# Optimization experiments

Measured on AMD Instinct MI355X. Metric: run time of the kernel, lower is better.

The kernel has to match this reference:

```python
import jax, jax.numpy as jnp
import numpy as np
from jax import lax

C = 256      # in_c == out_c == dim
NH = 8       # num_heads
K = 7        # depthwise pos-enc kernel
H1 = 512     # int(mlp_ratio * in_c) = 2.0 * 256
B, Hs, Ws = 2, 48, 48


def setup_inputs() -> dict:
    key = jax.random.key(0)
    ks = jax.random.split(key, 8)
    w = lambda k, shape: jax.random.normal(k, shape, jnp.float32) * 0.02
    return {
        "x": jax.random.normal(ks[0], (B, C, Hs, Ws), jnp.float32),
        # 1x1 convs stored as [out, in] (BN folded into weight+bias)
        "qk_w": w(ks[1], (2 * C, C)), "qk_b": jnp.zeros((2 * C,), jnp.float32),
        "v_w": w(ks[2], (C, C)),       "v_b": jnp.zeros((C,), jnp.float32),
        # depthwise positional encoding conv [C,1,K,K]
        "pe_w": w(ks[3], (C, 1, K, K)), "pe_b": jnp.zeros((C,), jnp.float32),
        "proj_w": w(ks[4], (C, C)),    "proj_b": jnp.zeros((C,), jnp.float32),
        # conv FFN: 1x1 (SiLU) -> 1x1 (no act)
        "fc1_w": w(ks[5], (H1, C)),    "fc1_b": jnp.zeros((H1,), jnp.float32),
        "fc2_w": w(ks[6], (C, H1)),    "fc2_b": jnp.zeros((C,), jnp.float32),
    }


def _c1(x, w, b):
    # 1x1 conv == per-pixel matmul
    return jnp.einsum('bchw,oc->bohw', x, w) + b[None, :, None, None]


def reference(x, qk_w, qk_b, v_w, v_b, pe_w, pe_b, proj_w, proj_b,
              fc1_w, fc1_b, fc2_w, fc2_b):
    Bb, Cc, Hh, Ww = x.shape
    hd = Cc // NH                 # head_dim = 32
    N = Hh * Ww
    scale = hd ** -0.5

    # ---- AttentionV2 ----
    qk = _c1(x, qk_w, qk_b).reshape(Bb, NH, 2 * hd, N)
    q, k = qk[:, :, :hd], qk[:, :, hd:]
    v_full = _c1(x, v_w, v_b)                      # [B,C,H,W]
    pe = lax.conv_general_dilated(
        v_full, pe_w, (1, 1), 'SAME', feature_group_count=Cc,
        dimension_numbers=('NCHW', 'OIHW', 'NCHW')) + pe_b[None, :, None, None]
    v = v_full.reshape(Bb, NH, hd, N)

    # attn = q^T @ k * scale ; softmax over keys
    attn = jax.nn.softmax(jnp.einsum('bhdn,bhdm->bhnm', q, k) * scale, axis=-1)
    o = jnp.einsum('bhdm,bhnm->bhdn', v, attn).reshape(Bb, Cc, Hh, Ww)
    attn_out = _c1(o + pe, proj_w, proj_b)

    # ---- block residuals + conv FFN (add=True) ----
    x1 = x + attn_out
    h = jax.nn.silu(_c1(x1, fc1_w, fc1_b))         # Conv(in_c, hidden, 1, 1) with SiLU
    return x1 + _c1(h, fc2_w, fc2_b)               # Conv(hidden, out_c, 1, act=False)
```

## Files before the change

### kernel.cpp

```cpp
#include <hip/hip_runtime.h>
#include <hip/hip_bf16.h>

#define NCH 256
#define NHD 8
#define HD 32
#define NPIX 2304
#define H1DIM 512

typedef __attribute__((ext_vector_type(8))) __bf16 bf16x8;
typedef __attribute__((ext_vector_type(4))) float f32x4;

__global__ __launch_bounds__(256) void prep_k(
    const float* __restrict__ x,
    const float* __restrict__ w0, const float* __restrict__ w1,
    const float* __restrict__ w2, const float* __restrict__ w3,
    const float* __restrict__ w4,
    __bf16* __restrict__ Xb, __bf16* __restrict__ Wall) {
    const int tid = threadIdx.x;
    if (blockIdx.x < 288) {
        const int t = blockIdx.x;
        const int b = t / 144, r0 = t % 144;
        const int c0 = (r0 / 36) * 64, n0 = (r0 % 36) * 64;
        __shared__ float tile[64][65];
        const size_t sb = ((size_t)b * NCH + c0) * NPIX + n0;
#pragma unroll
        for (int i = 0; i < 16; ++i) {
            int idx = tid + i * 256;
            int rr = idx >> 6, cc = idx & 63;
            tile[rr][cc] = x[sb + (size_t)rr * NPIX + cc];
        }
        __syncthreads();
#pragma unroll
        for (int i = 0; i < 8; ++i) {
            int idx = tid + i * 256;
            int nn = idx >> 5, cp = (idx & 31) * 2;
            union { __bf16 h[2]; unsigned u; } pk;
            pk.h[0] = (__bf16)tile[cp][nn];
            pk.h[1] = (__bf16)tile[cp + 1][nn];
            *(unsigned*)&Xb[((size_t)b * NPIX + n0 + nn) * NCH + c0 + cp] = pk.u;
        }
    } else {
        int i = (blockIdx.x - 288) * 256 + tid;
        const float* src; int off;
        if (i < 32768)      { src = w0; off = i; }
        else if (i < 49152) { src = w1; off = i - 32768; }
        else if (i < 65536) { src = w2; off = i - 49152; }
        else if (i < 98304) { src = w3; off = i - 65536; }
        else                { src = w4; off = i - 98304; }
        float4 v = ((const float4*)src)[off];
        union { __bf16 h[4]; uint2 u; } pk;
        pk.h[0] = (__bf16)v.x; pk.h[1] = (__bf16)v.y;
        pk.h[2] = (__bf16)v.z; pk.h[3] = (__bf16)v.w;
        ((uint2*)Wall)[i] = pk.u;
    }
}

__global__ __launch_bounds__(256) void qkv_k(
    const __bf16* __restrict__ A, const __bf16* __restrict__ Wq,
    const __bf16* __restrict__ Wv, const float* __restrict__ qk_b,
    const float* __restrict__ v_b, __bf16* __restrict__ Qb,
    __bf16* __restrict__ Kf, float* __restrict__ v_bu,
    __bf16* __restrict__ Vf) {
    const int tid = threadIdx.x;
    const int wave = tid >> 6, lane = tid & 63;
    const int l16 = lane & 15, quad = lane >> 4;
    const int h = blockIdx.x & 7;
    const int u = blockIdx.x >> 3;
    const int tau = u * 4 + wave;
    const int px = tau % 144;
    const int rest = tau / 144;
    const int b = rest & 1;
    const int sub = rest >> 1;
    const int m0 = px * 16;
    const bool isv = sub >= 4;
    const int oc0 = isv ? (32 * h + 16 * (sub - 4)) : (64 * h + 16 * sub);
    const __bf16* W = isv ? Wv : Wq;

    const __bf16* aptr = A + ((size_t)b * NPIX + m0 + l16) * NCH + quad * 8;
    const __bf16* bptr = W + (size_t)(oc0 + l16) * NCH + quad * 8;

    f32x4 acc = {0.f, 0.f, 0.f, 0.f};
#pragma unroll 8
    for (int k = 0; k < NCH; k += 32) {
        bf16x8 af = *(const bf16x8*)(aptr + k);
        bf16x8 bf = *(const bf16x8*)(bptr + k);
        acc = __builtin_amdgcn_mfma_f32_16x16x32_bf16(af, bf, acc, 0, 0, 0);
    }

    const int oc = oc0 + l16;
    const int mb = m0 + quad * 4;

    if (!isv) {
        const float bb = qk_b[oc];
        const int bh = b * NHD + h;
        const int dd = (oc0 & 16) + l16;
        if ((oc0 & 32) == 0) {
            const float qs = 0.17677669529663689f * 1.4426950408889634f;
#pragma unroll
            for (int r = 0; r < 4; ++r)
                Qb[((size_t)bh * NPIX + mb + r) * 32 + dd] = (__bf16)((acc[r] + bb) * qs);
        } else {
            __bf16* kp = Kf + ((size_t)(bh * 144 + px) * 64 + (dd >> 3) * 16 + quad * 4) * 8 + (dd & 7);
#pragma unroll
            for (int r = 0; r < 4; ++r) kp[r * 8] = (__bf16)(acc[r] + bb);
        }
    } else {
        const float bb = v_b[oc];
        const int bh = b * NHD + h;
        const int half = (oc0 >> 4) & 1;
        const size_t fb = ((size_t)b * NCH + oc) * NPIX + mb;
        float4 vf_; float* vp = &vf_.x;
        union { __bf16 hh[4]; uint2 u; } pk;
#pragma unroll
        for (int r = 0; r < 4; ++r) {
            float v = acc[r] + bb;
            vp[r] = v; pk.hh[r] = (__bf16)v;
        }
        *(float4*)&v_bu[fb] = vf_;
        *(uint2*)&Vf[((size_t)(bh * 144 + px) * 64 + lane) * 8 + half * 4] = pk.u;
    }
}

__global__ __launch_bounds__(256) void attn9_k(const __bf16* __restrict__ Qb,
                                               const __bf16* __restrict__ Kf,
                                               const __bf16* __restrict__ Vf,
                                               const float* __restrict__ v_bu,
                                               const float* __restrict__ pe_w,
                                               const float* __restrict__ pe_b,
                                               __bf16* __restrict__ opb) {
    const int tid = threadIdx.x;
    const int wave = tid >> 6, lane = tid & 63;
    const int l16 = lane & 15, quad = lane >> 4;
    const int h = blockIdx.x & 7;
    const int r0 = (int)blockIdx.x >> 3;
    const int qt = r0 % 72;
    const int b = r0 / 72;
    const int qb = qt * 32;
    const int bh = b * NHD + h;

    __shared__ float o_s[4][32][33];
    __shared__ float l_s[4][32];

    bf16x8 b_q0 = *(const bf16x8*)(Qb + ((size_t)bh * NPIX + qb + l16) * 32 + quad * 8);
    bf16x8 b_q1 = *(const bf16x8*)(Qb + ((size_t)bh * NPIX + qb + 16 + l16) * 32 + quad * 8);

    const __bf16* kf = Kf + ((size_t)(bh * 144 + wave * 36) * 64 + lane) * 8;
    const __bf16* vf = Vf + ((size_t)(bh * 144 + wave * 36) * 64 + lane) * 8;

    f32x4 o00 = {0.f,0.f,0.f,0.f}, o01 = {0.f,0.f,0.f,0.f};
    f32x4 o10 = {0.f,0.f,0.f,0.f}, o11 = {0.f,0.f,0.f,0.f};
    f32x4 l0 = {0.f,0.f,0.f,0.f}, l1 = {0.f,0.f,0.f,0.f};

#pragma unroll 3
    for (int t = 0; t < 36; ++t) {
        bf16x8 a_k = *(const bf16x8*)(kf + (size_t)t * 512);
        bf16x8 va  = *(const bf16x8*)(vf + (size_t)t * 512);
        f32x4 z = {0.f, 0.f, 0.f, 0.f};
        __builtin_amdgcn_s_setprio(1);
        f32x4 s0 = __builtin_amdgcn_mfma_f32_16x16x32_bf16(a_k, b_q0, z, 0, 0, 0);
        f32x4 s1 = __builtin_amdgcn_mfma_f32_16x16x32_bf16(a_k, b_q1, z, 0, 0, 0);
        __builtin_amdgcn_s_setprio(0);
        f32x4 p0, p1;
#pragma unroll
        for (int r = 0; r < 4; ++r) {
            p0[r] = __builtin_amdgcn_exp2f(s0[r]);
            p1[r] = __builtin_amdgcn_exp2f(s1[r]);
        }
        l0 += p0; l1 += p1;
        bf16x8 b0lo = {}, b0hi = {}, b1lo = {}, b1hi = {};
#pragma unroll
        for (int r = 0; r < 4; ++r) {
            __bf16 c0 = (__bf16)p0[r], c1 = (__bf16)p1[r];
            b0lo[r] = c0; b0hi[4 + r] = c0;
            b1lo[r] = c1; b1hi[4 + r] = c1;
        }
        __builtin_amdgcn_s_setprio(1);
        o00 = __builtin_amdgcn_mfma_f32_16x16x32_bf16(va, b0lo, o00, 0, 0, 0);
        o01 = __builtin_amdgcn_mfma_f32_16x16x32_bf16(va, b0hi, o01, 0, 0, 0);
        o10 = __builtin_amdgcn_mfma_f32_16x16x32_bf16(va, b1lo, o10, 0, 0, 0);
        o11 = __builtin_amdgcn_mfma_f32_16x16x32_bf16(va, b1hi, o11, 0, 0, 0);
        __builtin_amdgcn_s_setprio(0);
    }

    float ls0 = l0[0] + l0[1] + l0[2] + l0[3];
    ls0 += __shfl_xor(ls0, 16); ls0 += __shfl_xor(ls0, 32);
    float ls1 = l1[0] + l1[1] + l1[2] + l1[3];
    ls1 += __shfl_xor(ls1, 16); ls1 += __shfl_xor(ls1, 32);

#pragma unroll
    for (int r = 0; r < 4; ++r) {
        o_s[wave][quad * 4 + r][l16]           = o00[r];
        o_s[wave][16 + quad * 4 + r][l16]      = o01[r];
        o_s[wave][quad * 4 + r][16 + l16]      = o10[r];
        o_s[wave][16 + quad * 4 + r][16 + l16] = o11[r];
    }
    if (quad == 0) { l_s[wave][l16] = ls0; l_s[wave][16 + l16] = ls1; }
    __syncthreads();

    const int q = tid & 31;
    const int d0 = (tid >> 5) * 4;
    float l = l_s[0][q] + l_s[1][q] + l_s[2][q] + l_s[3][q];
    const float inv = 1.f / l;
    float v[4] = {0.f, 0.f, 0.f, 0.f};
#pragma unroll
    for (int w = 0; w < 4; ++w) {
#pragma unroll
        for (int j = 0; j < 4; ++j) v[j] += o_s[w][d0 + j][q];
    }
    const int n = qb + q;
    const int ch = h * HD + d0;

    const int y = n / 48, x0 = n - y * 48;
    const size_t vb0 = ((size_t)b * NCH + ch) * NPIX;
    float pe[4];
#pragma unroll
    for (int j = 0; j < 4; ++j) pe[j] = pe_b[ch + j];
#pragma unroll
    for (int ky = 0; ky < 7; ++ky) {
        int yy = y + ky - 3;
        if ((unsigned)yy < 48u) {
#pragma unroll
            for (int kx = 0; kx < 7; ++kx) {
                int xx = x0 + kx - 3;
                if ((unsigned)xx < 48u) {
                    const int off = yy * 48 + xx;
                    const int wko = ky * 7 + kx;
#pragma unroll
                    for (int j = 0; j < 4; ++j)
                        pe[j] += pe_w[(ch + j) * 49 + wko] * v_bu[vb0 + (size_t)j * NPIX + off];
                }
            }
        }
    }

    union { __bf16 hh[4]; uint2 u; } pk;
#pragma unroll
    for (int j = 0; j < 4; ++j) pk.hh[j] = (__bf16)(v[j] * inv + pe[j]);
    *(uint2*)&opb[((size_t)b * NPIX + n) * NCH + ch] = pk.u;
}

__global__ __launch_bounds__(512, 2) void mlp_k(
    const __bf16* __restrict__ opb, const __bf16* __restrict__ Wp,
    const __bf16* __restrict__ W1, const __bf16* __restrict__ W2,
    const float* __restrict__ pj_b, const float* __restrict__ f1_b,
    const float* __restrict__ f2_b, const float* __restrict__ x,
    float* __restrict__ out) {
    const int tid = threadIdx.x;
    const int wave = tid >> 6, lane = tid & 63;
    const int l16 = lane & 15, quad = lane >> 4;
    const int b = (int)blockIdx.x / 144;
    const int m0 = ((int)blockIdx.x % 144) * 16;

    __shared__ __bf16 x1h[16][264];
    __shared__ __bf16 hh[16][520];

    const int oc_a = wave * 16 + l16;
    const int oc_b = oc_a + 128;
    const int row = quad * 4;
    const int mq = m0 + quad * 4;

    const __bf16* aptr = opb + ((size_t)b * NPIX + m0 + l16) * NCH + quad * 8;
    const __bf16* wp0 = Wp + (size_t)oc_a * NCH + quad * 8;
    const __bf16* wp1 = Wp + (size_t)oc_b * NCH + quad * 8;
    f32x4 a0 = {0.f, 0.f, 0.f, 0.f}, a1 = {0.f, 0.f, 0.f, 0.f};
#pragma unroll
    for (int k = 0; k < NCH; k += 32) {
        bf16x8 af = *(const bf16x8*)(aptr + k);
        a0 = __builtin_amdgcn_mfma_f32_16x16x32_bf16(af, *(const bf16x8*)(wp0 + k), a0, 0, 0, 0);
        a1 = __builtin_amdgcn_mfma_f32_16x16x32_bf16(af, *(const bf16x8*)(wp1 + k), a1, 0, 0, 0);
    }
    float x1r0[4], x1r1[4];
    {
        const float bb0 = pj_b[oc_a], bb1 = pj_b[oc_b];
        float4 xr0 = *(const float4*)&x[((size_t)b * NCH + oc_a) * NPIX + mq];
        float4 xr1 = *(const float4*)&x[((size_t)b * NCH + oc_b) * NPIX + mq];
        const float* xp0 = &xr0.x;
        const float* xp1 = &xr1.x;
#pragma unroll
        for (int r = 0; r < 4; ++r) {
            float v0 = a0[r] + bb0 + xp0[r];
            float v1 = a1[r] + bb1 + xp1[r];
            x1r0[r] = v0; x1r1[r] = v1;
            x1h[row + r][oc_a] = (__bf16)v0;
            x1h[row + r][oc_b] = (__bf16)v1;
        }
    }
    __syncthreads();

    {
        const __bf16* w10 = W1 + (size_t)oc_a * NCH + quad * 8;
        const __bf16* w11 = W1 + (size_t)(oc_a + 128) * NCH + quad * 8;
        const __bf16* w12 = W1 + (size_t)(oc_a + 256) * NCH + quad * 8;
        const __bf16* w13 = W1 + (size_t)(oc_a + 384) * NCH + quad * 8;
        f32x4 c0 = {0.f, 0.f, 0.f, 0.f}, c1 = {0.f, 0.f, 0.f, 0.f};
        f32x4 c2 = {0.f, 0.f, 0.f, 0.f}, c3 = {0.f, 0.f, 0.f, 0.f};
#pragma unroll
        for (int k = 0; k < NCH; k += 32) {
            bf16x8 af = *(const bf16x8*)&x1h[l16][quad * 8 + k];
            c0 = __builtin_amdgcn_mfma_f32_16x16x32_bf16(af, *(const bf16x8*)(w10 + k), c0, 0, 0, 0);
            c1 = __builtin_amdgcn_mfma_f32_16x16x32_bf16(af, *(const bf16x8*)(w11 + k), c1, 0, 0, 0);
            c2 = __builtin_amdgcn_mfma_f32_16x16x32_bf16(af, *(const bf16x8*)(w12 + k), c2, 0, 0, 0);
            c3 = __builtin_amdgcn_mfma_f32_16x16x32_bf16(af, *(const bf16x8*)(w13 + k), c3, 0, 0, 0);
        }
        const float g0 = f1_b[oc_a], g1 = f1_b[oc_a + 128];
        const float g2 = f1_b[oc_a + 256], g3 = f1_b[oc_a + 384];
#pragma unroll
        for (int r = 0; r < 4; ++r) {
            float v0 = c0[r] + g0; v0 = v0 / (1.f + __expf(-v0));
            float v1 = c1[r] + g1; v1 = v1 / (1.f + __expf(-v1));
            float v2 = c2[r] + g2; v2 = v2 / (1.f + __expf(-v2));
            float v3 = c3[r] + g3; v3 = v3 / (1.f + __expf(-v3));
            hh[row + r][oc_a]       = (__bf16)v0;
            hh[row + r][oc_a + 128] = (__bf16)v1;
            hh[row + r][oc_a + 256] = (__bf16)v2;
            hh[row + r][oc_a + 384] = (__bf16)v3;
        }
    }
    __syncthreads();

    {
        const __bf16* w20 = W2 + (size_t)oc_a * H1DIM + quad * 8;
        const __bf16* w21 = W2 + (size_t)oc_b * H1DIM + quad * 8;
        f32x4 d0 = {0.f, 0.f, 0.f, 0.f}, d1 = {0.f, 0.f, 0.f, 0.f};
#pragma unroll
        for (int k = 0; k < H1DIM; k += 32) {
            bf16x8 af = *(const bf16x8*)&hh[l16][quad * 8 + k];
            d0 = __builtin_amdgcn_mfma_f32_16x16x32_bf16(af, *(const bf16x8*)(w20 + k), d0, 0, 0, 0);
            d1 = __builtin_amdgcn_mfma_f32_16x16x32_bf16(af, *(const bf16x8*)(w21 + k), d1, 0, 0, 0);
        }
        const float g0 = f2_b[oc_a], g1 = f2_b[oc_b];
        float4 o0, o1;
        float* p0 = &o0.x; float* p1 = &o1.x;
#pragma unroll
        for (int r = 0; r < 4; ++r) {
            p0[r] = d0[r] + g0 + x1r0[r];
            p1[r] = d1[r] + g1 + x1r1[r];
        }
        *(float4*)&out[((size_t)b * NCH + oc_a) * NPIX + mq] = o0;
        *(float4*)&out[((size_t)b * NCH + oc_b) * NPIX + mq] = o1;
    }
}

extern "C" void kernel_launch(void* const* d_in, const int* in_sizes, int n_in,
                              void* d_out, int out_size, void* d_ws, size_t ws_size,
                              hipStream_t stream) {
    const float* x    = (const float*)d_in[0];
    const float* qk_w = (const float*)d_in[1];
    const float* qk_b = (const float*)d_in[2];
    const float* v_w  = (const float*)d_in[3];
    const float* v_b  = (const float*)d_in[4];
    const float* pe_w = (const float*)d_in[5];
    const float* pe_b = (const float*)d_in[6];
    const float* pj_w = (const float*)d_in[7];
    const float* pj_b = (const float*)d_in[8];
    const float* f1_w = (const float*)d_in[9];
    const float* f1_b = (const float*)d_in[10];
    const float* f2_w = (const float*)d_in[11];
    const float* f2_b = (const float*)d_in[12];
    float* out = (float*)d_out;

    const int B = 2;
    const size_t plane = (size_t)NCH * NPIX;
    const size_t bp = (size_t)B * plane;

    float* v_bu  = (float*)d_ws;
    __bf16* Xb   = (__bf16*)(v_bu + bp);
    __bf16* opb  = Xb + bp;
    __bf16* Qb   = opb + bp;
    __bf16* Kf   = Qb + bp;
    __bf16* Vf   = Kf + bp;
    __bf16* Wall = Vf + bp;
    __bf16* Wq = Wall;
    __bf16* Wv = Wall + 131072;
    __bf16* Wp = Wall + 196608;
    __bf16* W1 = Wall + 262144;
    __bf16* W2 = Wall + 393216;

    prep_k<<<800, 256, 0, stream>>>(x, qk_w, v_w, pj_w, f1_w, f2_w, Xb, Wall);
    qkv_k<<<3456, 256, 0, stream>>>(Xb, Wq, Wv, qk_b, v_b, Qb, Kf, v_bu, Vf);
    attn9_k<<<1152, 256, 0, stream>>>(Qb, Kf, Vf, v_bu, pe_w, pe_b, opb);
    mlp_k<<<288, 512, 0, stream>>>(opb, Wp, W1, W2, pj_b, f1_b, f2_b, x, out);
}
```

Baseline: 190.0 us.

## Fuse input transpose and bf16 conversion into QKV projection kernel

Removes the separate prep kernel that transposed x into a pixel-major bf16 buffer. The QKV MFMA kernel now reads fp32 x and the fp32 qk/v weights directly, converting to bf16 in registers. Extra blocks appended to the same launch convert only the proj/fc1/fc2 weights for the MLP kernel. This saves a launch and an intermediate round trip, but the x loads are now strided by NPIX per element (16 consecutive pixels per lane group) and weights are re-read and re-converted redundantly by many blocks.

```diff
diff --git a/kernel.cpp b/kernel.cpp
--- a/kernel.cpp
+++ b/kernel.cpp
@@ -10,58 +10,29 @@
 typedef __attribute__((ext_vector_type(8))) __bf16 bf16x8;
 typedef __attribute__((ext_vector_type(4))) float f32x4;
 
-__global__ __launch_bounds__(256) void prep_k(
-    const float* __restrict__ x,
-    const float* __restrict__ w0, const float* __restrict__ w1,
-    const float* __restrict__ w2, const float* __restrict__ w3,
-    const float* __restrict__ w4,
-    __bf16* __restrict__ Xb, __bf16* __restrict__ Wall) {
+__global__ __launch_bounds__(256) void qkv2_k(
+    const float* __restrict__ x, const float* __restrict__ qk_w,
+    const float* __restrict__ v_w, const float* __restrict__ qk_b,
+    const float* __restrict__ v_b,
+    const float* __restrict__ pj_w, const float* __restrict__ f1_w,
+    const float* __restrict__ f2_w,
+    __bf16* __restrict__ Qb, __bf16* __restrict__ Kf,
+    float* __restrict__ v_bu, __bf16* __restrict__ Vf,
+    __bf16* __restrict__ Wall) {
     const int tid = threadIdx.x;
-    if (blockIdx.x < 288) {
-        const int t = blockIdx.x;
-        const int b = t / 144, r0 = t % 144;
-        const int c0 = (r0 / 36) * 64, n0 = (r0 % 36) * 64;
-        __shared__ float tile[64][65];
-        const size_t sb = ((size_t)b * NCH + c0) * NPIX + n0;
-#pragma unroll
-        for (int i = 0; i < 16; ++i) {
-            int idx = tid + i * 256;
-            int rr = idx >> 6, cc = idx & 63;
-            tile[rr][cc] = x[sb + (size_t)rr * NPIX + cc];
-        }
-        __syncthreads();
-#pragma unroll
-        for (int i = 0; i < 8; ++i) {
-            int idx = tid + i * 256;
-            int nn = idx >> 5, cp = (idx & 31) * 2;
-            union { __bf16 h[2]; unsigned u; } pk;
-            pk.h[0] = (__bf16)tile[cp][nn];
-            pk.h[1] = (__bf16)tile[cp + 1][nn];
-            *(unsigned*)&Xb[((size_t)b * NPIX + n0 + nn) * NCH + c0 + cp] = pk.u;
-        }
-    } else {
-        int i = (blockIdx.x - 288) * 256 + tid;
+    if (blockIdx.x >= 3456) {
+        int i = ((int)blockIdx.x - 3456) * 256 + tid;
         const float* src; int off;
-        if (i < 32768)      { src = w0; off = i; }
-        else if (i < 49152) { src = w1; off = i - 32768; }
-        else if (i < 65536) { src = w2; off = i - 49152; }
-        else if (i < 98304) { src = w3; off = i - 65536; }
-        else                { src = w4; off = i - 98304; }
+        if (i < 16384)      { src = pj_w; off = i; }
+        else if (i < 49152) { src = f1_w; off = i - 16384; }
+        else                { src = f2_w; off = i - 49152; }
         float4 v = ((const float4*)src)[off];
         union { __bf16 h[4]; uint2 u; } pk;
         pk.h[0] = (__bf16)v.x; pk.h[1] = (__bf16)v.y;
         pk.h[2] = (__bf16)v.z; pk.h[3] = (__bf16)v.w;
         ((uint2*)Wall)[i] = pk.u;
-    }
-}
-
-__global__ __launch_bounds__(256) void qkv_k(
-    const __bf16* __restrict__ A, const __bf16* __restrict__ Wq,
-    const __bf16* __restrict__ Wv, const float* __restrict__ qk_b,
-    const float* __restrict__ v_b, __bf16* __restrict__ Qb,
-    __bf16* __restrict__ Kf, float* __restrict__ v_bu,
-    __bf16* __restrict__ Vf) {
-    const int tid = threadIdx.x;
+        return;
+    }
     const int wave = tid >> 6, lane = tid & 63;
     const int l16 = lane & 15, quad = lane >> 4;
     const int h = blockIdx.x & 7;
@@ -74,16 +45,25 @@
     const int m0 = px * 16;
     const bool isv = sub >= 4;
     const int oc0 = isv ? (32 * h + 16 * (sub - 4)) : (64 * h + 16 * sub);
-    const __bf16* W = isv ? Wv : Wq;
-
-    const __bf16* aptr = A + ((size_t)b * NPIX + m0 + l16) * NCH + quad * 8;
-    const __bf16* bptr = W + (size_t)(oc0 + l16) * NCH + quad * 8;
+    const float* W32 = isv ? v_w : qk_w;
+
+    const float* xa = x + (size_t)b * NCH * NPIX + m0 + l16 + (size_t)(quad * 8) * NPIX;
+    const float* wp = W32 + (size_t)(oc0 + l16) * NCH + quad * 8;
 
     f32x4 acc = {0.f, 0.f, 0.f, 0.f};
-#pragma unroll 8
+#pragma unroll
     for (int k = 0; k < NCH; k += 32) {
-        bf16x8 af = *(const bf16x8*)(aptr + k);
-        bf16x8 bf = *(const bf16x8*)(bptr + k);
+        const float* xp = xa + (size_t)k * NPIX;
+        bf16x8 af;
+#pragma unroll
+        for (int j = 0; j < 8; ++j) af[j] = (__bf16)xp[(size_t)j * NPIX];
+        float4 w0 = *(const float4*)(wp + k);
+        float4 w1 = *(const float4*)(wp + k + 4);
+        bf16x8 bf;
+        bf[0] = (__bf16)w0.x; bf[1] = (__bf16)w0.y;
+        bf[2] = (__bf16)w0.z; bf[3] = (__bf16)w0.w;
+        bf[4] = (__bf16)w1.x; bf[5] = (__bf16)w1.y;
+        bf[6] = (__bf16)w1.z; bf[7] = (__bf16)w1.w;
         acc = __builtin_amdgcn_mfma_f32_16x16x32_bf16(af, bf, acc, 0, 0, 0);
     }
 
@@ -364,20 +344,17 @@
     const size_t bp = (size_t)B * plane;
 
     float* v_bu  = (float*)d_ws;
-    __bf16* Xb   = (__bf16*)(v_bu + bp);
-    __bf16* opb  = Xb + bp;
+    __bf16* opb  = (__bf16*)(v_bu + bp);
     __bf16* Qb   = opb + bp;
     __bf16* Kf   = Qb + bp;
     __bf16* Vf   = Kf + bp;
     __bf16* Wall = Vf + bp;
-    __bf16* Wq = Wall;
-    __bf16* Wv = Wall + 131072;
-    __bf16* Wp = Wall + 196608;
-    __bf16* W1 = Wall + 262144;
-    __bf16* W2 = Wall + 393216;
-
-    prep_k<<<800, 256, 0, stream>>>(x, qk_w, v_w, pj_w, f1_w, f2_w, Xb, Wall);
-    qkv_k<<<3456, 256, 0, stream>>>(Xb, Wq, Wv, qk_b, v_b, Qb, Kf, v_bu, Vf);
+    __bf16* Wp = Wall;
+    __bf16* W1 = Wall + 65536;
+    __bf16* W2 = Wall + 196608;
+
+    qkv2_k<<<3776, 256, 0, stream>>>(x, qk_w, v_w, qk_b, v_b, pj_w, f1_w, f2_w,
+                                     Qb, Kf, v_bu, Vf, Wall);
     attn9_k<<<1152, 256, 0, stream>>>(Qb, Kf, Vf, v_bu, pe_w, pe_b, opb);
     mlp_k<<<288, 512, 0, stream>>>(opb, Wp, W1, W2, pj_b, f1_b, f2_b, x, out);
 }
```

After: 199.1 us. 1.05x slower.
